# Performance work log

Measured on AMD Instinct MI355X. Metric: run time of the kernel, lower is better.

## Reference

```python
import jax, jax.numpy as jnp
import numpy as np

HIDDEN = 256
N_PROT = 12288
N_MOL = 6144
N_BATCH = 32


def setup_inputs() -> dict:
    key = jax.random.key(0)
    ks = jax.random.split(key, 10)
    s = 1.0 / np.sqrt(HIDDEN)  # torch Linear default init scale
    inp = {
        "prot_embed": jax.random.normal(ks[0], (N_PROT, HIDDEN), jnp.float32),
        "mol_embed": jax.random.normal(ks[1], (N_MOL, HIDDEN), jnp.float32),
        "prot_batch": jnp.sort(jax.random.randint(ks[2], (N_PROT,), 0, N_BATCH)),
        "mol_batch": jnp.sort(jax.random.randint(ks[3], (N_MOL,), 0, N_BATCH)),
        "Wq": jax.random.uniform(ks[4], (HIDDEN, HIDDEN), jnp.float32, -s, s),
        "bq": jax.random.uniform(ks[5], (HIDDEN,), jnp.float32, -s, s),
        "Wk": jax.random.uniform(ks[6], (HIDDEN, HIDDEN), jnp.float32, -s, s),
        "bk": jax.random.uniform(ks[7], (HIDDEN,), jnp.float32, -s, s),
        "Wv": jax.random.uniform(ks[8], (HIDDEN, HIDDEN), jnp.float32, -s, s),
        "bv": jax.random.uniform(ks[9], (HIDDEN,), jnp.float32, -s, s),
    }
    return inp


def reference(prot_embed, mol_embed, prot_batch, mol_batch, Wq, bq, Wk, bk, Wv, bv):
    # Linear projections (torch nn.Linear: x @ W.T + b)
    Q = prot_embed @ Wq.T + bq            # [N, H]
    K = mol_embed @ Wk.T + bk             # [M, H]
    V = mol_embed @ Wv.T + bv             # [M, H]

    scale = 1.0 / jnp.sqrt(jnp.asarray(Q.shape[-1], Q.dtype))
    scores = (Q @ K.T) * scale            # [N, M]

    # block mask: same-batch pairs only
    mask = prot_batch[:, None] == mol_batch[None, :]   # [N, M] bool
    neg_inf = jnp.asarray(-jnp.inf, scores.dtype)
    scores = jnp.where(mask, scores, neg_inf)

    # stable masked softmax; rows with no valid key -> all zeros
    # (matches torch softmax(-inf row) -> nan -> nan_to_num(0.0))
    row_any = mask.any(axis=-1, keepdims=True)
    mx = jnp.max(scores, axis=-1, keepdims=True)
    mx = jnp.where(row_any, mx, 0.0)
    e = jnp.exp(scores - mx)              # exp(-inf)=0 on masked entries
    denom = jnp.sum(e, axis=-1, keepdims=True)
    attn = e / jnp.where(row_any, denom, 1.0)  # [N, M]

    out = attn @ V                        # [N, H]
    return out, attn
```

## Files before the change

### kernel.cpp

```cpp
#include <hip/hip_runtime.h>

#define NPROT 12288
#define NMOL  6144
#define HID   256
#define NB    32

#define WQ_O   4718592
#define WK_O   4784128
#define WV_O   4849664
#define BQ_O   4915200
#define BK_O   4915456
#define BV_O   4915712
#define Q_O    4915968
#define K_O    8061696
#define VT_O   9634560
#define END_O  11207424

#define FROWS_BLK 49152

typedef __attribute__((ext_vector_type(4))) float f32x4;
typedef __attribute__((ext_vector_type(8))) short bf16x8;
typedef unsigned short u16;
typedef unsigned int   u32;

__device__ __forceinline__ float b2f(u16 u){
  union { u32 i; float f; } v; v.i = ((u32)u) << 16; return v.f;
}
__device__ __forceinline__ u16 f2b(float f){
  union { float fl; u32 i; } v; v.fl = f;
  u32 i = v.i;
  return (u16)((i + 0x7FFFu + ((i >> 16) & 1u)) >> 16);
}

__device__ __forceinline__ void fill_rows8(float* attnf, int fid){
  float* dst = attnf + (size_t)fid * FROWS_BLK + threadIdx.x * 4;
  f32x4 z = {0.f, 0.f, 0.f, 0.f};
  #pragma unroll 4
  for (int i = 0; i < 48; i++)
    __builtin_nontemporal_store(z, (f32x4*)(dst + i * 1024));
}

__global__ __launch_bounds__(256) void prep_kernel(
    const float* __restrict__ Wq, const float* __restrict__ Wk,
    const float* __restrict__ Wv, const float* __restrict__ bq,
    const float* __restrict__ bk, const float* __restrict__ bv,
    const int* __restrict__ pb, const int* __restrict__ mb,
    int* __restrict__ rg, u16* __restrict__ cvt, float* __restrict__ dout)
{
  if (blockIdx.x < 512){
    fill_rows8(dout + (size_t)NPROT * HID, blockIdx.x);
    return;
  }
  int g = (blockIdx.x - 512) * 256 + threadIdx.x;
  const float* src = nullptr; u16* dst = nullptr; int off = 0;
  if      (g < 16384) { src = Wq; dst = cvt + WQ_O; off = g; }
  else if (g < 32768) { src = Wk; dst = cvt + WK_O; off = g - 16384; }
  else if (g < 49152) { src = Wv; dst = cvt + WV_O; off = g - 32768; }
  else if (g < 49216) { src = bq; dst = cvt + BQ_O; off = g - 49152; }
  else if (g < 49280) { src = bk; dst = cvt + BK_O; off = g - 49216; }
  else if (g < 49344) { src = bv; dst = cvt + BV_O; off = g - 49280; }
  if (src){
    f32x4 v = *(const f32x4*)(src + (size_t)off * 4);
    ushort4 o;
    o.x = f2b(v[0]); o.y = f2b(v[1]); o.z = f2b(v[2]); o.w = f2b(v[3]);
    *(ushort4*)(dst + (size_t)off * 4) = o;
  }

  if (blockIdx.x == 512 && threadIdx.x < 64){
    int t = threadIdx.x;
    const int* arr = (t < 32) ? pb : mb;
    int n          = (t < 32) ? NPROT : NMOL;
    int target     = (t & 31) + 1;
    int lo = 0, hi = n;
    while (lo < hi){
      int mid = (lo + hi) >> 1;
      if (arr[mid] < target) lo = mid + 1; else hi = mid;
    }
    int end = lo;
    int prev = __shfl(end, t - 1);
    int start = ((t & 31) == 0) ? 0 : prev;
    int b = t & 31;
    if (t < 32){ rg[b] = start; rg[32 + b] = end; }
    else       { rg[64 + b] = start; rg[96 + b] = end; }
  }
}

__global__ __launch_bounds__(256) void proj_kernel(
    const float* __restrict__ prot, const float* __restrict__ mol,
    const u16* __restrict__ cvt,
    u16* __restrict__ Q, u16* __restrict__ K, u16* __restrict__ Vt,
    float* __restrict__ dout)
{
  __shared__ u16 xlds[16][264];
  __shared__ u16 tlds[4][64][18];
  if (blockIdx.x >= 1536){
    fill_rows8(dout + (size_t)NPROT * HID, blockIdx.x - 1536 + 512);
    return;
  }
  int rb = blockIdx.x;
  int proj;
  const float* X; const u16 *W, *B;
  if      (rb < 768) { proj = 0; X = prot; W = cvt + WQ_O; B = cvt + BQ_O; }
  else if (rb < 1152){ proj = 1; rb -= 768;  X = mol; W = cvt + WK_O; B = cvt + BK_O; }
  else               { proj = 2; rb -= 1152; X = mol; W = cvt + WV_O; B = cvt + BV_O; }
  int rowbase = rb * 16;

  {
    int r  = threadIdx.x >> 4;
    int c0 = (threadIdx.x & 15) * 16;
    const float* xp = X + (size_t)(rowbase + r) * HID + c0;
    f32x4 v0 = *(const f32x4*)(xp);
    f32x4 v1 = *(const f32x4*)(xp + 4);
    f32x4 v2 = *(const f32x4*)(xp + 8);
    f32x4 v3 = *(const f32x4*)(xp + 12);
    u16* d = &xlds[r][c0];
    ushort4 o0, o1, o2, o3;
    o0.x = f2b(v0[0]); o0.y = f2b(v0[1]); o0.z = f2b(v0[2]); o0.w = f2b(v0[3]);
    o1.x = f2b(v1[0]); o1.y = f2b(v1[1]); o1.z = f2b(v1[2]); o1.w = f2b(v1[3]);
    o2.x = f2b(v2[0]); o2.y = f2b(v2[1]); o2.z = f2b(v2[2]); o2.w = f2b(v2[3]);
    o3.x = f2b(v3[0]); o3.y = f2b(v3[1]); o3.z = f2b(v3[2]); o3.w = f2b(v3[3]);
    *(ushort4*)(d)      = o0;
    *(ushort4*)(d + 4)  = o1;
    *(ushort4*)(d + 8)  = o2;
    *(ushort4*)(d + 12) = o3;
  }
  __syncthreads();

  int wave = threadIdx.x >> 6, lane = threadIdx.x & 63;
  int m = lane & 15, q = lane >> 4;
  int colbase = wave * 64;

  f32x4 acc[4] = {};
  for (int k0 = 0; k0 < HID; k0 += 32){
    bf16x8 a = *(const bf16x8*)(&xlds[m][k0 + q*8]);
    #pragma unroll
    for (int ct = 0; ct < 4; ct++){
      bf16x8 b = *(const bf16x8*)(W + (size_t)(colbase + ct*16 + m) * HID + k0 + q*8);
      acc[ct] = __builtin_amdgcn_mfma_f32_16x16x32_bf16(a, b, acc[ct], 0, 0, 0);
    }
  }

  if (proj < 2){
    u16* O = (proj == 0) ? Q : K;
    #pragma unroll
    for (int ct = 0; ct < 4; ct++){
      int col = colbase + ct*16 + m;
      float bb = b2f(B[col]);
      #pragma unroll
      for (int r = 0; r < 4; r++){
        int row = rowbase + q*4 + r;
        O[(size_t)row * HID + col] = f2b(acc[ct][r] + bb);
      }
    }
  } else {
    #pragma unroll
    for (int ct = 0; ct < 4; ct++){
      int lc = ct*16 + m;
      float bb = b2f(B[colbase + lc]);
      #pragma unroll
      for (int r = 0; r < 4; r++)
        tlds[wave][lc][q*4 + r] = f2b(acc[ct][r] + bb);
    }
    __syncthreads();
    int col = colbase + lane;
    u32 packed[8];
    #pragma unroll
    for (int i = 0; i < 8; i++){
      u16 lo = tlds[wave][lane][2*i];
      u16 hi = tlds[wave][lane][2*i+1];
      packed[i] = (u32)lo | ((u32)hi << 16);
    }
    u16* dst = Vt + (size_t)col * NMOL + rowbase;
    uint4 v0 = {packed[0], packed[1], packed[2], packed[3]};
    uint4 v1 = {packed[4], packed[5], packed[6], packed[7]};
    *(uint4*)dst = v0;
    *(uint4*)(dst + 8) = v1;
  }
}

__global__ __launch_bounds__(256) void attn_kernel(
    const int* __restrict__ rg, const int* __restrict__ pb,
    const u16* __restrict__ Q, const u16* __restrict__ K,
    const u16* __restrict__ Vt, float* __restrict__ dout)
{
  __shared__ u16 P[16][392];
  __shared__ float mxw[4][16];
  __shared__ float smw[4][16];
  const float scale = 0.0625f;
  float* outf  = dout;
  float* attnf = dout + (size_t)NPROT * HID;

  if (blockIdx.x >= 32){
    int fid = (blockIdx.x - 32) + 8 * blockIdx.y;
    int r0 = 8192 + fid * 16;
    f32x4 z = {0.f, 0.f, 0.f, 0.f};
    for (int rr = 0; rr < 16; rr++){
      int row = r0 + rr;
      int bb = pb[row];
      int ms = rg[64 + bb], me = rg[96 + bb];
      float* rowp = attnf + (size_t)row * NMOL;
      int mv = ms & ~3;
      for (int c = threadIdx.x * 4; c < mv; c += 1024)
        __builtin_nontemporal_store(z, (f32x4*)(rowp + c));
      for (int c = mv + threadIdx.x; c < ms; c += 256)
        rowp[c] = 0.f;
      int mu = (me + 3) & ~3;
      for (int c = me + threadIdx.x; c < mu && c < NMOL; c += 256)
        rowp[c] = 0.f;
      for (int c = mu + threadIdx.x * 4; c < NMOL; c += 1024)
        __builtin_nontemporal_store(z, (f32x4*)(rowp + c));
    }
    return;
  }

  int b = blockIdx.y;
  int ps = rg[b], pe = rg[32+b], ms = rg[64+b], me = rg[96+b];
  int Np = pe - ps, Nm = me - ms;
  if (Np <= 0) return;

  int wave = threadIdx.x >> 6, lane = threadIdx.x & 63;
  int m = lane & 15, q = lane >> 4;
  int ntiles = (Np + 15) >> 4;

  int bs = 0, ce = 0;
  if (Nm > 0){ bs = ms & ~31; ce = bs + ((me - bs + 31) & ~31); }

  for (int tile = blockIdx.x; tile < ntiles; tile += 32){
    int row0 = ps + tile * 16;
    int qr = min(row0 + m, NPROT - 1);
    const u16* qrow = Q + (size_t)qr * HID;
    bf16x8 qf[8];
    #pragma unroll
    for (int kk = 0; kk < 8; kk++)
      qf[kk] = *(const bf16x8*)(qrow + kk*32 + q*8);

    if (Nm > 0){
      int myj0 = bs + wave * 16;
      f32x4 sreg[6];
      float mx[4] = {-1e30f, -1e30f, -1e30f, -1e30f};
      #pragma unroll
      for (int c = 0; c < 6; c++){
        int j0 = myj0 + 64*c;
        if (j0 < ce){
          int col = j0 + m;
          bool valid = (col >= ms) && (col < me);
          const u16* krow = K + (size_t)col * HID;
          f32x4 s0 = {0.f,0.f,0.f,0.f}, s1 = {0.f,0.f,0.f,0.f};
          #pragma unroll
          for (int kk = 0; kk < 4; kk++){
            bf16x8 kb0 = *(const bf16x8*)(krow + kk*32 + q*8);
            bf16x8 kb1 = *(const bf16x8*)(krow + (kk+4)*32 + q*8);
            s0 = __builtin_amdgcn_mfma_f32_16x16x32_bf16(qf[kk],   kb0, s0, 0, 0, 0);
            s1 = __builtin_amdgcn_mfma_f32_16x16x32_bf16(qf[kk+4], kb1, s1, 0, 0, 0);
          }
          f32x4 sv;
          #pragma unroll
          for (int r = 0; r < 4; r++)
            sv[r] = valid ? (s0[r] + s1[r]) * scale : -1e30f;
          sreg[c] = sv;
          float cm[4];
          #pragma unroll
          for (int r = 0; r < 4; r++) cm[r] = sv[r];
          #pragma unroll
          for (int d = 1; d < 16; d <<= 1)
            #pragma unroll
            for (int r = 0; r < 4; r++)
              cm[r] = fmaxf(cm[r], __shfl_xor(cm[r], d, 16));
          #pragma unroll
          for (int r = 0; r < 4; r++) mx[r] = fmaxf(mx[r], cm[r]);
        }
      }
      if (m == 0){
        #pragma unroll
        for (int r = 0; r < 4; r++) mxw[wave][q*4 + r] = mx[r];
      }
      __syncthreads();
      float gmx[4];
      #pragma unroll
      for (int r = 0; r < 4; r++){
        int row = q*4 + r;
        float M = mxw[0][row];
        #pragma unroll
        for (int w = 1; w < 4; w++) M = fmaxf(M, mxw[w][row]);
        gmx[r] = M;
      }

      float sm[4] = {0.f, 0.f, 0.f, 0.f};
      #pragma unroll
      for (int c = 0; c < 6; c++){
        int j0 = myj0 + 64*c;
        if (j0 < ce){
          f32x4 e;
          #pragma unroll
          for (int r = 0; r < 4; r++) e[r] = __expf(sreg[c][r] - gmx[r]);
          sreg[c] = e;
          float t[4];
          #pragma unroll
          for (int r = 0; r < 4; r++) t[r] = e[r];
          #pragma unroll
          for (int d = 1; d < 16; d <<= 1)
            #pragma unroll
            for (int r = 0; r < 4; r++)
              t[r] += __shfl_xor(t[r], d, 16);
          #pragma unroll
          for (int r = 0; r < 4; r++) sm[r] += t[r];
        }
      }
      if (m == 0){
        #pragma unroll
        for (int r = 0; r < 4; r++) smw[wave][q*4 + r] = sm[r];
      }
      __syncthreads();
      float ginv[4];
      #pragma unroll
      for (int r = 0; r < 4; r++){
        int row = q*4 + r;
        float S = smw[0][row] + smw[1][row] + smw[2][row] + smw[3][row];
        ginv[r] = (S > 0.f) ? (1.f / S) : 0.f;
      }

      #pragma unroll
      for (int c = 0; c < 6; c++){
        int j0 = myj0 + 64*c;
        if (j0 < ce){
          int col = j0 + m;
          int jl = j0 - bs;
          bool valid = (col >= ms) && (col < me);
          #pragma unroll
          for (int r = 0; r < 4; r++){
            float p = sreg[c][r] * ginv[r];
            P[q*4 + r][jl + m] = f2b(p);
            int row = row0 + q*4 + r;
            if (valid && row < pe)
              __builtin_nontemporal_store(p, attnf + (size_t)row * NMOL + col);
          }
        }
      }
      __syncthreads();

      f32x4 oacc[4] = {};
      for (int j0 = bs; j0 < ce; j0 += 32){
        int jl = j0 - bs;
        bf16x8 a = *(const bf16x8*)(&P[m][jl + q*8]);
        #pragma unroll
        for (int c2 = 0; c2 < 4; c2++){
          int ct = wave*4 + c2;
          bf16x8 vb = *(const bf16x8*)(Vt + (size_t)(ct*16 + m) * NMOL + j0 + q*8);
          oacc[c2] = __builtin_amdgcn_mfma_f32_16x16x32_bf16(a, vb, oacc[c2], 0, 0, 0);
        }
      }
      #pragma unroll
      for (int c2 = 0; c2 < 4; c2++){
        int col = (wave*4 + c2)*16 + m;
        #pragma unroll
        for (int r = 0; r < 4; r++){
          int row = row0 + q*4 + r;
          if (row < pe) outf[(size_t)row * HID + col] = oacc[c2][r];
        }
      }
    } else {
      #pragma unroll
      for (int c2 = 0; c2 < 4; c2++){
        int col = (wave*4 + c2)*16 + m;
        #pragma unroll
        for (int r = 0; r < 4; r++){
          int row = row0 + q*4 + r;
          if (row < pe) outf[(size_t)row * HID + col] = 0.f;
        }
      }
    }
    __syncthreads();
  }
}

extern "C" void kernel_launch(void* const* d_in, const int* in_sizes, int n_in,
                              void* d_out, int out_size, void* d_ws, size_t ws_size,
                              hipStream_t stream)
{
  (void)in_sizes; (void)n_in; (void)out_size;
  const float* prot = (const float*)d_in[0];
  const float* mol  = (const float*)d_in[1];
  const int* pb     = (const int*)d_in[2];
  const int* mb     = (const int*)d_in[3];
  const float* Wq   = (const float*)d_in[4];
  const float* bq   = (const float*)d_in[5];
  const float* Wk   = (const float*)d_in[6];
  const float* bk   = (const float*)d_in[7];
  const float* Wv   = (const float*)d_in[8];
  const float* bv   = (const float*)d_in[9];

  const size_t need = 1024 + (size_t)END_O * 2;
  if (ws_size < need) return;

  char* ws = (char*)d_ws;
  int* rg  = (int*)ws;
  u16* cvt = (u16*)(ws + 1024);
  u16* Qp  = cvt + Q_O;
  u16* Kp  = cvt + K_O;
  u16* Vtp = cvt + VT_O;
  float* out = (float*)d_out;

  prep_kernel<<<dim3(512 + 193), dim3(256), 0, stream>>>(
      Wq, Wk, Wv, bq, bk, bv, pb, mb, rg, cvt, out);
  proj_kernel<<<dim3(1536 + 512), dim3(256), 0, stream>>>(
      prot, mol, cvt, Qp, Kp, Vtp, out);
  attn_kernel<<<dim3(40, NB), dim3(256), 0, stream>>>(rg, pb, Qp, Kp, Vtp, out);
}
```

Before: 390.9 us.

## Give each wave its own row tile and recompute scores to drop block syncs

Restructures the attention kernel so each wave handles 16 query rows independently over all key columns, computing max, sum and final probabilities in three passes that recompute QK^T instead of storing scores. This removes the cross-wave LDS reductions and __syncthreads barriers, and each wave computes all 256 output columns. It trades extra MFMA work and K reloads plus higher register use for removing synchronization; the grid's compute portion shrinks accordingly.

```diff
diff --git a/kernel.cpp b/kernel.cpp
--- a/kernel.cpp
+++ b/kernel.cpp
@@ -183,15 +183,13 @@
     const u16* __restrict__ Q, const u16* __restrict__ K,
     const u16* __restrict__ Vt, float* __restrict__ dout)
 {
-  __shared__ u16 P[16][392];
-  __shared__ float mxw[4][16];
-  __shared__ float smw[4][16];
+  __shared__ u16 P[4][16][392];
   const float scale = 0.0625f;
   float* outf  = dout;
   float* attnf = dout + (size_t)NPROT * HID;
 
-  if (blockIdx.x >= 32){
-    int fid = (blockIdx.x - 32) + 8 * blockIdx.y;
+  if (blockIdx.x >= 8){
+    int fid = (blockIdx.x - 8) + 8 * blockIdx.y;
     int r0 = 8192 + fid * 16;
     f32x4 z = {0.f, 0.f, 0.f, 0.f};
     for (int rr = 0; rr < 16; rr++){
@@ -220,13 +218,20 @@
 
   int wave = threadIdx.x >> 6, lane = threadIdx.x & 63;
   int m = lane & 15, q = lane >> 4;
-  int ntiles = (Np + 15) >> 4;
-
-  int bs = 0, ce = 0;
-  if (Nm > 0){ bs = ms & ~31; ce = bs + ((me - bs + 31) & ~31); }
-
-  for (int tile = blockIdx.x; tile < ntiles; tile += 32){
-    int row0 = ps + tile * 16;
+
+  int bs = 0, S = 0;
+  if (Nm > 0){
+    bs = ms & ~31;
+    int ce = bs + ((me - bs + 31) & ~31);
+    S = (ce - bs) >> 4;
+    if (S > 24) S = 24;
+  }
+  u16 (*Pw)[392] = P[wave];
+
+  for (int rb = blockIdx.x; rb * 64 < Np; rb += 8){
+    int row0 = ps + rb * 64 + wave * 16;
+    if (row0 >= pe) continue;
+
     int qr = min(row0 + m, NPROT - 1);
     const u16* qrow = Q + (size_t)qr * HID;
     bf16x8 qf[8];
@@ -234,142 +239,106 @@
     for (int kk = 0; kk < 8; kk++)
       qf[kk] = *(const bf16x8*)(qrow + kk*32 + q*8);
 
-    if (Nm > 0){
-      int myj0 = bs + wave * 16;
-      f32x4 sreg[6];
-      float mx[4] = {-1e30f, -1e30f, -1e30f, -1e30f};
-      #pragma unroll
-      for (int c = 0; c < 6; c++){
-        int j0 = myj0 + 64*c;
-        if (j0 < ce){
-          int col = j0 + m;
-          bool valid = (col >= ms) && (col < me);
-          const u16* krow = K + (size_t)col * HID;
-          f32x4 s0 = {0.f,0.f,0.f,0.f}, s1 = {0.f,0.f,0.f,0.f};
-          #pragma unroll
-          for (int kk = 0; kk < 4; kk++){
-            bf16x8 kb0 = *(const bf16x8*)(krow + kk*32 + q*8);
-            bf16x8 kb1 = *(const bf16x8*)(krow + (kk+4)*32 + q*8);
-            s0 = __builtin_amdgcn_mfma_f32_16x16x32_bf16(qf[kk],   kb0, s0, 0, 0, 0);
-            s1 = __builtin_amdgcn_mfma_f32_16x16x32_bf16(qf[kk+4], kb1, s1, 0, 0, 0);
-          }
-          f32x4 sv;
-          #pragma unroll
-          for (int r = 0; r < 4; r++)
-            sv[r] = valid ? (s0[r] + s1[r]) * scale : -1e30f;
-          sreg[c] = sv;
-          float cm[4];
-          #pragma unroll
-          for (int r = 0; r < 4; r++) cm[r] = sv[r];
-          #pragma unroll
-          for (int d = 1; d < 16; d <<= 1)
-            #pragma unroll
-            for (int r = 0; r < 4; r++)
-              cm[r] = fmaxf(cm[r], __shfl_xor(cm[r], d, 16));
-          #pragma unroll
-          for (int r = 0; r < 4; r++) mx[r] = fmaxf(mx[r], cm[r]);
-        }
-      }
-      if (m == 0){
+    float mw[4] = {-1e30f, -1e30f, -1e30f, -1e30f};
+    for (int s = 0; s < S; s++){
+      int col = bs + s*16 + m;
+      bool valid = (col >= ms) && (col < me);
+      const u16* krow = K + (size_t)col * HID;
+      f32x4 s0 = {0.f,0.f,0.f,0.f}, s1 = {0.f,0.f,0.f,0.f};
+      #pragma unroll
+      for (int kk = 0; kk < 4; kk++){
+        bf16x8 kb0 = *(const bf16x8*)(krow + kk*32 + q*8);
+        bf16x8 kb1 = *(const bf16x8*)(krow + (kk+4)*32 + q*8);
+        s0 = __builtin_amdgcn_mfma_f32_16x16x32_bf16(qf[kk],   kb0, s0, 0, 0, 0);
+        s1 = __builtin_amdgcn_mfma_f32_16x16x32_bf16(qf[kk+4], kb1, s1, 0, 0, 0);
+      }
+      float cm[4];
+      #pragma unroll
+      for (int r = 0; r < 4; r++)
+        cm[r] = valid ? (s0[r] + s1[r]) * scale : -1e30f;
+      #pragma unroll
+      for (int d = 1; d < 16; d <<= 1)
         #pragma unroll
-        for (int r = 0; r < 4; r++) mxw[wave][q*4 + r] = mx[r];
-      }
-      __syncthreads();
-      float gmx[4];
+        for (int r = 0; r < 4; r++)
+          cm[r] = fmaxf(cm[r], __shfl_xor(cm[r], d, 16));
+      #pragma unroll
+      for (int r = 0; r < 4; r++) mw[r] = fmaxf(mw[r], cm[r]);
+    }
+
+    float sm[4] = {0.f, 0.f, 0.f, 0.f};
+    for (int s = 0; s < S; s++){
+      int col = bs + s*16 + m;
+      bool valid = (col >= ms) && (col < me);
+      const u16* krow = K + (size_t)col * HID;
+      f32x4 s0 = {0.f,0.f,0.f,0.f}, s1 = {0.f,0.f,0.f,0.f};
+      #pragma unroll
+      for (int kk = 0; kk < 4; kk++){
+        bf16x8 kb0 = *(const bf16x8*)(krow + kk*32 + q*8);
+        bf16x8 kb1 = *(const bf16x8*)(krow + (kk+4)*32 + q*8);
+        s0 = __builtin_amdgcn_mfma_f32_16x16x32_bf16(qf[kk],   kb0, s0, 0, 0, 0);
+        s1 = __builtin_amdgcn_mfma_f32_16x16x32_bf16(qf[kk+4], kb1, s1, 0, 0, 0);
+      }
+      float t[4];
       #pragma unroll
       for (int r = 0; r < 4; r++){
-        int row = q*4 + r;
-        float M = mxw[0][row];
+        float sv = valid ? (s0[r] + s1[r]) * scale : -1e30f;
+        t[r] = __expf(sv - mw[r]);
+      }
+      #pragma unroll
+      for (int d = 1; d < 16; d <<= 1)
         #pragma unroll
-        for (int w = 1; w < 4; w++) M = fmaxf(M, mxw[w][row]);
-        gmx[r] = M;
-      }
-
-      float sm[4] = {0.f, 0.f, 0.f, 0.f};
-      #pragma unroll
-      for (int c = 0; c < 6; c++){
-        int j0 = myj0 + 64*c;
-        if (j0 < ce){
-          f32x4 e;
-          #pragma unroll
-          for (int r = 0; r < 4; r++) e[r] = __expf(sreg[c][r] - gmx[r]);
-          sreg[c] = e;
-          float t[4];
-          #pragma unroll
-          for (int r = 0; r < 4; r++) t[r] = e[r];
-          #pragma unroll
-          for (int d = 1; d < 16; d <<= 1)
-            #pragma unroll
-            for (int r = 0; r < 4; r++)
-              t[r] += __shfl_xor(t[r], d, 16);
-          #pragma unroll
-          for (int r = 0; r < 4; r++) sm[r] += t[r];
-        }
-      }
-      if (m == 0){
-        #pragma unroll
-        for (int r = 0; r < 4; r++) smw[wave][q*4 + r] = sm[r];
-      }
-      __syncthreads();
-      float ginv[4];
+        for (int r = 0; r < 4; r++)
+          t[r] += __shfl_xor(t[r], d, 16);
+      #pragma unroll
+      for (int r = 0; r < 4; r++) sm[r] += t[r];
+    }
+    float ginv[4];
+    #pragma unroll
+    for (int r = 0; r < 4; r++)
+      ginv[r] = (sm[r] > 0.f) ? (1.f / sm[r]) : 0.f;
+
+    for (int s = 0; s < S; s++){
+      int jl = s*16;
+      int col = bs + jl + m;
+      bool valid = (col >= ms) && (col < me);
+      const u16* krow = K + (size_t)col * HID;
+      f32x4 s0 = {0.f,0.f,0.f,0.f}, s1 = {0.f,0.f,0.f,0.f};
+      #pragma unroll
+      for (int kk = 0; kk < 4; kk++){
+        bf16x8 kb0 = *(const bf16x8*)(krow + kk*32 + q*8);
+        bf16x8 kb1 = *(const bf16x8*)(krow + (kk+4)*32 + q*8);
+        s0 = __builtin_amdgcn_mfma_f32_16x16x32_bf16(qf[kk],   kb0, s0, 0, 0, 0);
+        s1 = __builtin_amdgcn_mfma_f32_16x16x32_bf16(qf[kk+4], kb1, s1, 0, 0, 0);
+      }
       #pragma unroll
       for (int r = 0; r < 4; r++){
-        int row = q*4 + r;
-        float S = smw[0][row] + smw[1][row] + smw[2][row] + smw[3][row];
-        ginv[r] = (S > 0.f) ? (1.f / S) : 0.f;
-      }
-
-      #pragma unroll
-      for (int c = 0; c < 6; c++){
-        int j0 = myj0 + 64*c;
-        if (j0 < ce){
-          int col = j0 + m;
-          int jl = j0 - bs;
-          bool valid = (col >= ms) && (col < me);
-          #pragma unroll
-          for (int r = 0; r < 4; r++){
-            float p = sreg[c][r] * ginv[r];
-            P[q*4 + r][jl + m] = f2b(p);
-            int row = row0 + q*4 + r;
-            if (valid && row < pe)
-              __builtin_nontemporal_store(p, attnf + (size_t)row * NMOL + col);
-          }
-        }
-      }
-      __syncthreads();
-
-      f32x4 oacc[4] = {};
-      for (int j0 = bs; j0 < ce; j0 += 32){
-        int jl = j0 - bs;
-        bf16x8 a = *(const bf16x8*)(&P[m][jl + q*8]);
-        #pragma unroll
-        for (int c2 = 0; c2 < 4; c2++){
-          int ct = wave*4 + c2;
-          bf16x8 vb = *(const bf16x8*)(Vt + (size_t)(ct*16 + m) * NMOL + j0 + q*8);
-          oacc[c2] = __builtin_amdgcn_mfma_f32_16x16x32_bf16(a, vb, oacc[c2], 0, 0, 0);
-        }
-      }
-      #pragma unroll
-      for (int c2 = 0; c2 < 4; c2++){
-        int col = (wave*4 + c2)*16 + m;
-        #pragma unroll
-        for (int r = 0; r < 4; r++){
-          int row = row0 + q*4 + r;
-          if (row < pe) outf[(size_t)row * HID + col] = oacc[c2][r];
-        }
-      }
-    } else {
-      #pragma unroll
-      for (int c2 = 0; c2 < 4; c2++){
-        int col = (wave*4 + c2)*16 + m;
-        #pragma unroll
-        for (int r = 0; r < 4; r++){
-          int row = row0 + q*4 + r;
-          if (row < pe) outf[(size_t)row * HID + col] = 0.f;
-        }
-      }
-    }
-    __syncthreads();
+        float sv = valid ? (s0[r] + s1[r]) * scale : -1e30f;
+        float p = __expf(sv - mw[r]) * ginv[r];
+        Pw[q*4 + r][jl + m] = f2b(p);
+        int row = row0 + q*4 + r;
+        if (valid && row < pe)
+          __builtin_nontemporal_store(p, attnf + (size_t)row * NMOL + col);
+      }
+    }
+
+    f32x4 oacc[16] = {};
+    for (int jl = 0; jl < S*16; jl += 32){
+      bf16x8 a = *(const bf16x8*)(&Pw[m][jl + q*8]);
+      #pragma unroll
+      for (int c2 = 0; c2 < 16; c2++){
+        bf16x8 vb = *(const bf16x8*)(Vt + (size_t)(c2*16 + m) * NMOL + bs + jl + q*8);
+        oacc[c2] = __builtin_amdgcn_mfma_f32_16x16x32_bf16(a, vb, oacc[c2], 0, 0, 0);
+      }
+    }
+    #pragma unroll
+    for (int c2 = 0; c2 < 16; c2++){
+      int col = c2*16 + m;
+      #pragma unroll
+      for (int r = 0; r < 4; r++){
+        int row = row0 + q*4 + r;
+        if (row < pe) outf[(size_t)row * HID + col] = oacc[c2][r];
+      }
+    }
   }
 }
 
@@ -404,5 +373,5 @@
       Wq, Wk, Wv, bq, bk, bv, pb, mb, rg, cvt, out);
   proj_kernel<<<dim3(1536 + 512), dim3(256), 0, stream>>>(
       prot, mol, cvt, Qp, Kp, Vtp, out);
-  attn_kernel<<<dim3(40, NB), dim3(256), 0, stream>>>(rg, pb, Qp, Kp, Vtp, out);
-}
+  attn_kernel<<<dim3(16, NB), dim3(256), 0, stream>>>(rg, pb, Qp, Kp, Vtp, out);
+}
```

New measurement: 474.0 us. 1.21x slower.
